# Kernel optimization log

Measured on AMD Instinct MI355X. Metric: run time of the kernel, lower is better.

The kernel has to match this reference:

```python
import jax, jax.numpy as jnp
import numpy as np

NH = 8          # attention heads
NC = 14         # disease classes
K = 10          # aspect queries per class
E = 1024        # vision_dim == text_dim
HID = 512       # hidden_dim = vision_dim // 2
TEMP = 0.1
LN_EPS = 1e-5


def _layernorm(x, g, b):
    m = jnp.mean(x, axis=-1, keepdims=True)
    v = jnp.mean(jnp.square(x - m), axis=-1, keepdims=True)
    return (x - m) * jax.lax.rsqrt(v + LN_EPS) * g + b


def _mha(q, k, v, in_w, in_b, out_w, out_b):
    # nn.MultiheadAttention (batch_first, eval mode => dropout off)
    B, Lq, Emb = q.shape
    Lk = k.shape[1]
    dh = Emb // NH
    wq, wk, wv = jnp.split(in_w, 3, axis=0)
    bq, bk, bv = jnp.split(in_b, 3)
    qh = (q @ wq.T + bq).reshape(B, Lq, NH, dh)
    kh = (k @ wk.T + bk).reshape(B, Lk, NH, dh)
    vh = (v @ wv.T + bv).reshape(B, Lk, NH, dh)
    scale = np.float32(1.0 / np.sqrt(dh))
    scores = jnp.einsum('bqhd,bkhd->bhqk', qh, kh) * scale
    attn = jax.nn.softmax(scores, axis=-1)
    out = jnp.einsum('bhqk,bkhd->bqhd', attn, vh).reshape(B, Lq, Emb)
    out = out @ out_w.T + out_b
    return out, attn.mean(axis=1)  # avg over heads, (B, Lq, Lk)


def _l2norm(x):
    return x / jnp.maximum(jnp.linalg.norm(x, axis=-1, keepdims=True), 1e-12)


def reference(vision_features, text_embeddings, vision_global, aspect_queries,
              ch_in_w, ch_in_b, ch_out_w, ch_out_b, tp_w, tp_b,
              ca_in_w, ca_in_b, ca_out_w, ca_out_b,
              cross_ln_g, cross_ln_b, cross_fc_w, cross_fc_b,
              dir_ln_g, dir_ln_b, dir_w1, dir_b1, dir_w2, dir_b2):
    B, N, _ = vision_features.shape
    # ---- contrastive branch (1-token query / 1-token kv attention) ----
    text_proj = text_embeddings @ tp_w.T + tp_b               # (B, E)
    c_out, _ = _mha(vision_global[:, None, :], text_proj[:, None, :],
                    text_proj[:, None, :], ch_in_w, ch_in_b, ch_out_w, ch_out_b)
    sim = jnp.sum(_l2norm(c_out[:, 0, :]) * _l2norm(text_proj), axis=-1) / TEMP  # (B,)
    contrastive_logits = jnp.broadcast_to(sim[:, None], (B, NC))
    # ---- supervised branch: fused per-class cross-attention (shared K/V) ----
    q = jnp.broadcast_to(aspect_queries.reshape(1, NC * K, E), (B, NC * K, E))
    att_out, attn_w = _mha(q, vision_features, vision_features,
                           ca_in_w, ca_in_b, ca_out_w, ca_out_b)
    attended = att_out.reshape(B, NC, K, E).mean(axis=2)       # (B, NC, E)
    attention_weights = attn_w.reshape(B, NC, K, N)            # (B, NC, K, N)
    # fc_cross: LN + per-class linear row (class j feature -> class j logit)
    h = _layernorm(attended, cross_ln_g, cross_ln_b)
    logits_cross = jnp.einsum('bjd,jd->bj', h, cross_fc_w) + cross_fc_b
    # fc_direct MLP on global feature
    g = _layernorm(vision_global, dir_ln_g, dir_ln_b)
    logits_direct = jax.nn.relu(g @ dir_w1.T + dir_b1) @ dir_w2.T + dir_b2
    supervised_logits = (logits_cross + logits_direct) * 0.5
    final_logits = (supervised_logits + contrastive_logits) * 0.5
    return contrastive_logits, supervised_logits, final_logits, attention_weights


def setup_inputs() -> dict:
    key = jax.random.key(0)
    ks = jax.random.split(key, 16)
    B, N = 64, 576
    w = lambda k, s: (jax.random.normal(k, s, dtype=jnp.float32) * 0.02)
    return {
        'vision_features': jax.random.normal(ks[0], (B, N, E), dtype=jnp.float32),
        'text_embeddings': jax.random.normal(ks[1], (B, E), dtype=jnp.float32),
        'vision_global': jax.random.normal(ks[2], (B, E), dtype=jnp.float32),
        'aspect_queries': jax.random.normal(ks[3], (NC, K, E), dtype=jnp.float32) / np.sqrt(E).astype(np.float32),
        'ch_in_w': w(ks[4], (3 * E, E)), 'ch_in_b': jnp.zeros((3 * E,), jnp.float32),
        'ch_out_w': w(ks[5], (E, E)), 'ch_out_b': jnp.zeros((E,), jnp.float32),
        'tp_w': w(ks[6], (E, E)), 'tp_b': jnp.zeros((E,), jnp.float32),
        'ca_in_w': w(ks[7], (3 * E, E)), 'ca_in_b': jnp.zeros((3 * E,), jnp.float32),
        'ca_out_w': w(ks[8], (E, E)), 'ca_out_b': jnp.zeros((E,), jnp.float32),
        'cross_ln_g': jnp.ones((E,), jnp.float32), 'cross_ln_b': jnp.zeros((E,), jnp.float32),
        'cross_fc_w': w(ks[9], (NC, E)), 'cross_fc_b': jnp.zeros((NC,), jnp.float32),
        'dir_ln_g': jnp.ones((E,), jnp.float32), 'dir_ln_b': jnp.zeros((E,), jnp.float32),
        'dir_w1': w(ks[10], (HID, E)), 'dir_b1': jnp.zeros((HID,), jnp.float32),
        'dir_w2': w(ks[11], (NC, HID)), 'dir_b2': jnp.zeros((NC,), jnp.float32),
    }
```

## Files before the change

kernel.cpp:

```cpp
#include <hip/hip_runtime.h>
#include <cstdio>
#include <cstdint>

using u16 = unsigned short;
typedef __bf16 bf16x8 __attribute__((ext_vector_type(8)));
typedef float f32x4 __attribute__((ext_vector_type(4)));

#define GLOBAL_AS __attribute__((address_space(1)))
#define LDS_AS __attribute__((address_space(3)))

__device__ __forceinline__ float bf2f(u16 h) {
  return __uint_as_float(((unsigned)h) << 16);
}
__device__ __forceinline__ u16 f2bf(float f) {
  unsigned u = __float_as_uint(f);
  u += 0x7FFFu + ((u >> 16) & 1u);
  return (u16)(u >> 16);
}

__device__ __forceinline__ void async_copy16(void* lds, const void* g) {
  __builtin_amdgcn_global_load_lds((const GLOBAL_AS unsigned int*)g,
                                   (LDS_AS unsigned int*)lds, 16, 0, 0);
}

__device__ __forceinline__ float block_sum(float v, float* red) {
#pragma unroll
  for (int o = 32; o >= 1; o >>= 1) v += __shfl_xor(v, o);
  __syncthreads();
  if ((threadIdx.x & 63) == 0) red[threadIdx.x >> 6] = v;
  __syncthreads();
  return red[0] + red[1] + red[2] + red[3];
}

__global__ __launch_bounds__(256) void cvt4_kernel(
    const float* __restrict__ s0, u16* __restrict__ d0,
    const float* __restrict__ s1, u16* __restrict__ d1,
    const float* __restrict__ s2, u16* __restrict__ d2,
    const float* __restrict__ s3, u16* __restrict__ d3) {
  const float* s; u16* d; long n; long b0; long nb;
  const int b = blockIdx.x;
  if (b < 2048)      { s = s0; d = d0; n = 37748736L; b0 = b;        nb = 2048; }
  else if (b < 2816) { s = s1; d = d1; n = 3145728L;  b0 = b - 2048; nb = 768; }
  else if (b < 3072) { s = s2; d = d2; n = 1048576L;  b0 = b - 2816; nb = 256; }
  else               { s = s3; d = d3; n = 143360L;   b0 = b - 3072; nb = 35; }
  long i = (b0 * 256 + threadIdx.x) * 4;
  const long stride = nb * 1024;
  for (; i < n; i += stride) {
    float4 v = *(const float4*)(s + i);
    ushort4 o;
    o.x = f2bf(v.x); o.y = f2bf(v.y); o.z = f2bf(v.z); o.w = f2bf(v.w);
    *(ushort4*)(d + i) = o;
  }
}

template <int VTD>
__global__ __launch_bounds__(512, 2) void gemm_kvq_kernel(
    const u16* __restrict__ A, const u16* __restrict__ Bkv,
    const u16* __restrict__ Aq, const u16* __restrict__ Bq,
    u16* __restrict__ Ck, u16* __restrict__ Cvp, u16* __restrict__ Vt,
    u16* __restrict__ Cq,
    const float* __restrict__ bias, const float* __restrict__ biasq) {
  __shared__ char smem[131072];
  const int bid = blockIdx.x;
  const int t = threadIdx.x;
  const int wid = t >> 6, l = t & 63;
  const int wm = wid >> 2, wn = wid & 3;
  const int lr = l & 15, lg = l >> 4, lr7 = lr & 7;

  int mt = 0, nt = 0, qb = -1;
  const u16* Abase; const u16* Bbase; const float* bias_b;
  if (bid < 1152) {
    const int wgid = (bid & 7) * 144 + (bid >> 3);
    mt = wgid >> 3; nt = wgid & 7;
    Abase = A + (size_t)mt * 256 * 1024;
    Bbase = Bkv + (size_t)nt * 256 * 1024;
    bias_b = bias + nt * 256;
  } else {
    qb = bid - 1152;
    Abase = Aq;
    Bbase = Bq + (size_t)qb * 256 * 1024;
    bias_b = biasq + qb * 256;
  }

  const int srow = t >> 3;
  const int scx = (t & 7) ^ (srow & 7);
  const char* Asrc = (const char*)Abase + (size_t)srow * 2048 + (scx << 4);
  const char* Bsrc = (const char*)Bbase + (size_t)srow * 2048 + (scx << 4);
  const int wb = wid << 10;

  f32x4 acc[8][4] = {};

#define SA(d, r, kt) async_copy16(smem + (d)*65536 + (r)*8192 + wb, \
                                  Asrc + (size_t)(r)*131072 + (size_t)(kt)*128)
#define SB(d, r, kt) async_copy16(smem + (d)*65536 + 32768 + (r)*8192 + wb, \
                                  Bsrc + (size_t)(r)*131072 + (size_t)(kt)*128)

#define RA(d, half)                                                          \
  _Pragma("unroll")                                                          \
  for (int i = 0; i < 4; ++i) {                                              \
    const int row = wm * 128 + ((half)*4 + i) * 16 + lr;                     \
    af[i][0] = *(const bf16x8*)(smem + (d)*65536 + (row << 7) + ((lg ^ lr7) << 4));       \
    af[i][1] = *(const bf16x8*)(smem + (d)*65536 + (row << 7) + (((4 | lg) ^ lr7) << 4)); \
  }

#define RB(d, half)                                                          \
  _Pragma("unroll")                                                          \
  for (int j = 0; j < 2; ++j) {                                              \
    const int row = wn * 64 + ((half)*2 + j) * 16 + lr;                      \
    bfr[j][0] = *(const bf16x8*)(smem + (d)*65536 + 32768 + (row << 7) + ((lg ^ lr7) << 4));       \
    bfr[j][1] = *(const bf16x8*)(smem + (d)*65536 + 32768 + (row << 7) + (((4 | lg) ^ lr7) << 4)); \
  }

#define MM(mh, nh)                                                           \
  __builtin_amdgcn_s_setprio(1);                                             \
  _Pragma("unroll")                                                          \
  for (int ks = 0; ks < 2; ++ks)                                             \
    _Pragma("unroll")                                                        \
    for (int i = 0; i < 4; ++i)                                              \
      _Pragma("unroll")                                                      \
      for (int j = 0; j < 2; ++j)                                            \
        acc[(mh)*4 + i][(nh)*2 + j] = __builtin_amdgcn_mfma_f32_16x16x32_bf16( \
            af[i][ks], bfr[j][ks], acc[(mh)*4 + i][(nh)*2 + j], 0, 0, 0);    \
  __builtin_amdgcn_s_setprio(0);

  SA(0, 0, 0); SA(0, 1, 0); SA(0, 2, 0); SA(0, 3, 0);
  SB(0, 0, 0); SB(0, 1, 0); SB(0, 2, 0); SB(0, 3, 0);
  SA(1, 0, 1); SA(1, 2, 1);
  asm volatile("s_waitcnt vmcnt(2)" ::: "memory");
  __builtin_amdgcn_s_barrier();
  asm volatile("" ::: "memory");

#pragma unroll 1
  for (int kt = 0; kt < 16; ++kt) {
    const int cur = kt & 1, nxt = cur ^ 1;
    const bool pf1 = (kt < 15), pf2 = (kt < 14);
    bf16x8 af[4][2], bfr[2][2];
    RA(cur, 0);
    RB(cur, 0);
    if (pf1) { SB(nxt, 0, kt + 1); SB(nxt, 1, kt + 1); }
    __builtin_amdgcn_s_barrier();
    asm volatile("s_waitcnt lgkmcnt(0)" ::: "memory");
    MM(0, 0);
    __builtin_amdgcn_s_barrier();
    RB(cur, 1);
    if (pf1) { SB(nxt, 2, kt + 1); SB(nxt, 3, kt + 1); }
    __builtin_amdgcn_s_barrier();
    asm volatile("s_waitcnt lgkmcnt(0)" ::: "memory");
    MM(0, 1);
    if (pf1) asm volatile("s_waitcnt vmcnt(6)" ::: "memory");
    __builtin_amdgcn_s_barrier();
    RA(cur, 1);
    if (pf1) { SA(nxt, 1, kt + 1); SA(nxt, 3, kt + 1); }
    __builtin_amdgcn_s_barrier();
    asm volatile("s_waitcnt lgkmcnt(0)" ::: "memory");
    MM(1, 1);
    __builtin_amdgcn_s_barrier();
    RB(cur, 0);
    if (pf2) { SA(cur, 0, kt + 2); SA(cur, 2, kt + 2); }
    __builtin_amdgcn_s_barrier();
    asm volatile("s_waitcnt lgkmcnt(0)" ::: "memory");
    MM(1, 0);
    if (pf2)      asm volatile("s_waitcnt vmcnt(4)" ::: "memory");
    else if (pf1) asm volatile("s_waitcnt vmcnt(0)" ::: "memory");
    __builtin_amdgcn_s_barrier();
  }
#undef SA
#undef SB
#undef RA
#undef RB
#undef MM

  if (VTD && qb < 0 && nt >= 4) {
    u16* T = (u16*)smem;
    const int vc2 = t >> 1, seg = t & 1;
    const int vglob = (nt - 4) * 256 + vc2;
    const int h2 = vglob >> 7, d2 = vglob & 127;
#pragma unroll 1
    for (int mh = 0; mh < 2; ++mh) {
      __syncthreads();
      if (wm == mh) {
#pragma unroll
        for (int ni = 0; ni < 4; ++ni) {
          const int vc = wn * 64 + ni * 16 + lr;
          const float bv = bias_b[vc];
#pragma unroll
          for (int mi = 0; mi < 8; ++mi) {
            const int ml = mi * 16 + lg * 4;
            ushort4 pk;
            pk.x = f2bf(acc[mi][ni][0] + bv);
            pk.y = f2bf(acc[mi][ni][1] + bv);
            pk.z = f2bf(acc[mi][ni][2] + bv);
            pk.w = f2bf(acc[mi][ni][3] + bv);
            *(ushort4*)(T + (size_t)vc * 136 + ml) = pk;
          }
        }
      }
      __syncthreads();
      const int mg0 = mt * 256 + mh * 128 + seg * 64;
      const int bb = (unsigned)mg0 / 576u;
      const int k0 = mg0 - bb * 576;
      u16* dst = Vt + ((size_t)(bb * 8 + h2) * 128 + d2) * 576 + k0;
      const u16* src = T + (size_t)vc2 * 136 + seg * 64;
#pragma unroll
      for (int i2 = 0; i2 < 8; ++i2)
        *(uint4*)(dst + i2 * 8) = *(const uint4*)(src + i2 * 8);
    }
  } else {
    u16* D; int cb0;
    if (qb >= 0)      { D = Cq;  cb0 = qb * 256; }
    else if (nt < 4)  { D = Ck;  cb0 = nt * 256; }
    else              { D = Cvp; cb0 = (nt - 4) * 256; }
#pragma unroll
    for (int ni = 0; ni < 4; ++ni) {
      const int nc = wn * 64 + ni * 16 + lr;
      const float bv = bias_b[nc];
      const int col = cb0 + nc;
#pragma unroll
      for (int mi = 0; mi < 8; ++mi) {
#pragma unroll
        for (int rg = 0; rg < 4; ++rg) {
          const size_t m = (size_t)mt * 256 + wm * 128 + mi * 16 + lg * 4 + rg;
          D[m * 1024 + col] = f2bf(acc[mi][ni][rg] + bv);
        }
      }
    }
  }
}

template <int OUTF32>
__global__ __launch_bounds__(512, 2) void gemm_big_kernel(
    const u16* __restrict__ A, const u16* __restrict__ B, void* __restrict__ Cv,
    const float* __restrict__ bias, float scale,
    int KT, int ntx, int Mlim, int Nlim,
    long lda, long ldb, long ldc, int bdiv,
    long sA0, long sA1, long sB0, long sB1, long sC0, long sC1) {
  __shared__ u16 lds[3][24576];
  const int bid = blockIdx.x;
  const int bh = blockIdx.y;
  const int bb0 = bh / bdiv, bb1 = bh % bdiv;
  const int mt = bid / ntx, nt = bid % ntx;
  const int t = threadIdx.x;
  const int wid = t >> 6, l = t & 63;
  const int wr = wid >> 1, wc = wid & 1;
  const int lr = l & 15, lg = l >> 4, lr7 = lr & 7;

  const long ldab = lda * 2, ldbb = ldb * 2;
  const u16* Abase = A + (long)bb0 * sA0 + (long)bb1 * sA1 + (long)mt * 256 * lda;
  const u16* Bbase = B + (long)bb0 * sB0 + (long)bb1 * sB1 + (long)nt * 128 * ldb;

  const int srow = t >> 3;
  const int scx = (t & 7) ^ (srow & 7);
  const char* Asrc = (const char*)Abase + (long)srow * ldab + (scx << 4);
  const char* Bsrc = (const char*)Bbase + (long)srow * ldbb + (scx << 4);
  const int wbA = wid << 10;

  char* b0 = (char*)lds[0];
  char* b1 = (char*)lds[1];
  char* b2 = (char*)lds[2];

  f32x4 acc[4][4] = {};

#define STAGE3G(dst, kt, part)                                              \
  {                                                                         \
    const long ko = (long)(kt) * 128;                                       \
    if ((part) == 0) {                                                      \
      async_copy16((dst) + wbA,          Asrc + ko);                        \
      async_copy16((dst) + 8192 + wbA,   Asrc + 64 * ldab + ko);            \
      async_copy16((dst) + 16384 + wbA,  Asrc + 128 * ldab + ko);           \
    } else {                                                                \
      async_copy16((dst) + 24576 + wbA,  Asrc + 192 * ldab + ko);           \
      async_copy16((dst) + 32768 + wbA,  Bsrc + ko);                        \
      async_copy16((dst) + 40960 + wbA,  Bsrc + 64 * ldbb + ko);            \
    }                                                                       \
  }

#define COMPUTE_KS(p, KS)                                                   \
  {                                                                         \
    const int ccol = (((KS) << 2) | lg) ^ lr7;                              \
    const char* pA = (p) + (((wr << 6) + lr) << 7) + (ccol << 4);           \
    const char* pB = (p) + 32768 + (((wc << 6) + lr) << 7) + (ccol << 4);   \
    bf16x8 af[4], bfr[4];                                                   \
    _Pragma("unroll")                                                       \
    for (int i = 0; i < 4; ++i) {                                           \
      af[i]  = *(const bf16x8*)(pA + i * 2048);                             \
      bfr[i] = *(const bf16x8*)(pB + i * 2048);                             \
    }                                                                       \
    __builtin_amdgcn_s_setprio(1);                                          \
    _Pragma("unroll")                                                       \
    for (int mi = 0; mi < 4; ++mi)                                          \
      _Pragma("unroll")                                                     \
      for (int ni = 0; ni < 4; ++ni)                                        \
        acc[mi][ni] = __builtin_amdgcn_mfma_f32_16x16x32_bf16(              \
            af[mi], bfr[ni], acc[mi][ni], 0, 0, 0);                         \
    __builtin_amdgcn_s_setprio(0);                                          \
  }

  STAGE3G(b0, 0, 0); STAGE3G(b0, 0, 1);
  STAGE3G(b1, 1, 0); STAGE3G(b1, 1, 1);
  asm volatile("s_waitcnt vmcnt(6)" ::: "memory");
  __builtin_amdgcn_s_barrier();
  asm volatile("" ::: "memory");

  char* p0 = b0; char* p1 = b1; char* p2 = b2;
#pragma unroll 1
  for (int kt = 0; kt < KT; ++kt) {
    const bool pf = (kt < KT - 2);
    if (pf) STAGE3G(p2, kt + 2, 0);
    COMPUTE_KS(p0, 0);
    if (pf) STAGE3G(p2, kt + 2, 1);
    COMPUTE_KS(p0, 1);
    if (kt < KT - 1) {
      if (pf) asm volatile("s_waitcnt vmcnt(6)" ::: "memory");
      else    asm volatile("s_waitcnt vmcnt(0)" ::: "memory");
      __builtin_amdgcn_s_barrier();
      asm volatile("" ::: "memory");
    }
    char* tmp = p0; p0 = p1; p1 = p2; p2 = tmp;
  }
#undef STAGE3G
#undef COMPUTE_KS

  const long cBase = (long)bb0 * sC0 + (long)bb1 * sC1;
  const int mr0 = mt * 256 + wr * 64 + lg * 4;
  const int nc0 = nt * 128 + wc * 64 + lr;
#pragma unroll
  for (int ni = 0; ni < 4; ++ni) {
    const int n = nc0 + ni * 16;
    if (n >= Nlim) continue;
    const float bv = bias ? bias[n] : 0.0f;
#pragma unroll
    for (int mi = 0; mi < 4; ++mi) {
#pragma unroll
      for (int rg = 0; rg < 4; ++rg) {
        const int m = mr0 + mi * 16 + rg;
        if (m >= Mlim) continue;
        const float v = acc[mi][ni][rg] * scale + bv;
        if (OUTF32) ((float*)Cv)[cBase + (long)m * ldc + n] = v;
        else        ((u16*)Cv)[cBase + (long)m * ldc + n] = f2bf(v);
      }
    }
  }
}

__global__ __launch_bounds__(256) void transpose_v_kernel(const u16* __restrict__ V,
                                                          u16* __restrict__ Vt) {
  __shared__ u16 tile[64][65];
  const int k0 = blockIdx.x * 64;
  const int c0 = blockIdx.y * 64;
  const int b = blockIdx.z;
  const int t = threadIdx.x;
  const int tx = t & 15, ty = t >> 4;
  const u16* Vb = V + (size_t)(b * 576) * 1024;
#pragma unroll
  for (int i = 0; i < 4; ++i) {
    const int k = ty + i * 16;
    const u16* src = Vb + (size_t)(k0 + k) * 1024 + c0 + tx * 4;
    ushort2 v01 = *(const ushort2*)src;
    ushort2 v23 = *(const ushort2*)(src + 2);
    tile[k][tx * 4 + 0] = v01.x; tile[k][tx * 4 + 1] = v01.y;
    tile[k][tx * 4 + 2] = v23.x; tile[k][tx * 4 + 3] = v23.y;
  }
  __syncthreads();
  const int h = c0 >> 7, d0 = c0 & 127;
  u16* VtB = Vt + ((size_t)(b * 8 + h) * 128 + d0) * 576 + k0;
#pragma unroll
  for (int i = 0; i < 4; ++i) {
    const int d = ty + i * 16;
    u16* dst = VtB + (size_t)d * 576 + tx * 4;
    ushort2 a, bb2;
    a.x = tile[tx * 4 + 0][d]; a.y = tile[tx * 4 + 1][d];
    bb2.x = tile[tx * 4 + 2][d]; bb2.y = tile[tx * 4 + 3][d];
    *(ushort2*)dst = a; *(ushort2*)(dst + 2) = bb2;
  }
}

__global__ __launch_bounds__(512) void softmax_pm_kernel(const u16* __restrict__ SP,
                                                         float* __restrict__ attnOut,
                                                         u16* __restrict__ Pm) {
  const int b = blockIdx.x, c = blockIdx.y;
  const int h = threadIdx.x >> 6, l = threadIdx.x & 63;
  __shared__ float pl[8][576];
  float pacc[9] = {};
#pragma unroll 1
  for (int qq = 0; qq < 10; ++qq) {
    const u16* row = SP + ((size_t)((b * 8 + h) * 144 + c * 10 + qq)) * 576;
    float x[9];
#pragma unroll
    for (int i = 0; i < 9; ++i) x[i] = bf2f(row[l + 64 * i]);
    float m = x[0];
#pragma unroll
    for (int i = 1; i < 9; ++i) m = fmaxf(m, x[i]);
#pragma unroll
    for (int o = 32; o >= 1; o >>= 1) m = fmaxf(m, __shfl_xor(m, o));
    float e[9], s = 0.f;
#pragma unroll
    for (int i = 0; i < 9; ++i) { e[i] = expf(x[i] - m); s += e[i]; }
#pragma unroll
    for (int o = 32; o >= 1; o >>= 1) s += __shfl_xor(s, o);
    const float inv = 1.f / s;
#pragma unroll
    for (int i = 0; i < 9; ++i) {
      const float p = e[i] * inv;
      pacc[i] += p;
      pl[h][l + 64 * i] = p;
    }
    __syncthreads();
    float* out = attnOut + ((size_t)(b * 140 + c * 10 + qq)) * 576;
    {
      const int j = threadIdx.x;
      float a = 0.f;
#pragma unroll
      for (int hh = 0; hh < 8; ++hh) a += pl[hh][j];
      out[j] = a * 0.125f;
      if (j < 64) {
        float a2 = 0.f;
#pragma unroll
        for (int hh = 0; hh < 8; ++hh) a2 += pl[hh][j + 512];
        out[j + 512] = a2 * 0.125f;
      }
    }
    __syncthreads();
  }
  u16* pm = Pm + ((size_t)((b * 8 + h) * 14 + c)) * 576;
#pragma unroll
  for (int i = 0; i < 9; ++i) pm[l + 64 * i] = f2bf(pacc[i] * 0.1f);
}

__global__ __launch_bounds__(128) void pv_small_kernel(const u16* __restrict__ Pm,
                                                       const u16* __restrict__ Vt,
                                                       u16* __restrict__ Attd) {
  const int b = blockIdx.x, hq = blockIdx.y;
  const int t = threadIdx.x;
  const int w = t >> 6, l = t & 63;
  const int h = hq * 2 + w;
  const int lr = l & 15, lg = l >> 4;
  __shared__ u16 pm[2][16][584];
  for (int i = t; i < 2336; i += 128) {
    const int hh = i / 1168;
    const int rem = i - hh * 1168;
    const int r = rem / 73, ck = rem - (rem / 73) * 73;
    uint4 v = {0u, 0u, 0u, 0u};
    if (r < 14 && ck < 72)
      v = *(const uint4*)&Pm[((size_t)((b * 8 + hq * 2 + hh) * 14 + r)) * 576 + ck * 8];
    *(uint4*)&pm[hh][r][ck * 8] = v;
  }
  __syncthreads();
  const u16* vbase = Vt + ((size_t)(b * 8 + h) * 128) * 576;
  f32x4 acc[8] = {};
#pragma unroll 1
  for (int ks = 0; ks < 18; ++ks) {
    const bf16x8 af = *(const bf16x8*)&pm[w][lr][ks * 32 + lg * 8];
#pragma unroll
    for (int nf = 0; nf < 8; ++nf) {
      const bf16x8 bf = *(const bf16x8*)&vbase[(size_t)(nf * 16 + lr) * 576 + ks * 32 + lg * 8];
      acc[nf] = __builtin_amdgcn_mfma_f32_16x16x32_bf16(af, bf, acc[nf], 0, 0, 0);
    }
  }
#pragma unroll
  for (int nf = 0; nf < 8; ++nf) {
#pragma unroll
    for (int rg = 0; rg < 4; ++rg) {
      const int cc = lg * 4 + rg;
      if (cc < 14)
        Attd[((size_t)b * 14 + cc) * 1024 + h * 128 + nf * 16 + lr] = f2bf(acc[nf][rg]);
    }
  }
}

__global__ __launch_bounds__(256) void ln_crossfc_kernel(
    const float* __restrict__ ap, const float* __restrict__ g, const float* __restrict__ bb,
    const float* __restrict__ fw, const float* __restrict__ fb, float* __restrict__ out) {
  const int bc = blockIdx.x;
  const int c = bc % 14;
  const float* x = ap + (size_t)bc * 1024;
  __shared__ float red[4];
  const int t = threadIdx.x;
  float v[4];
  float s = 0.f;
#pragma unroll
  for (int i = 0; i < 4; ++i) { v[i] = x[t + i * 256]; s += v[i]; }
  const float mean = block_sum(s, red) * (1.f / 1024.f);
  float vs = 0.f;
#pragma unroll
  for (int i = 0; i < 4; ++i) { const float d = v[i] - mean; vs += d * d; }
  const float var = block_sum(vs, red) * (1.f / 1024.f);
  const float inv = rsqrtf(var + 1e-5f);
  float acc = 0.f;
#pragma unroll
  for (int i = 0; i < 4; ++i) {
    const int e = t + i * 256;
    const float h = (v[i] - mean) * inv * g[e] + bb[e];
    acc += h * fw[(size_t)c * 1024 + e];
  }
  acc = block_sum(acc, red);
  if (t == 0) out[bc] = acc + fb[c];
}

__global__ __launch_bounds__(256) void direct_mlp_kernel(
    const float* __restrict__ vg, const float* __restrict__ g, const float* __restrict__ bb,
    const float* __restrict__ w1, const float* __restrict__ b1,
    const float* __restrict__ w2, const float* __restrict__ b2, float* __restrict__ out) {
  const int b = blockIdx.x;
  __shared__ float red[4];
  __shared__ float gn[1024];
  __shared__ float h1[512];
  const int t = threadIdx.x;
  const float* x = vg + (size_t)b * 1024;
  float v[4];
  float s = 0.f;
#pragma unroll
  for (int i = 0; i < 4; ++i) { v[i] = x[t + i * 256]; s += v[i]; }
  const float mean = block_sum(s, red) * (1.f / 1024.f);
  float vs = 0.f;
#pragma unroll
  for (int i = 0; i < 4; ++i) { const float d = v[i] - mean; vs += d * d; }
  const float var = block_sum(vs, red) * (1.f / 1024.f);
  const float inv = rsqrtf(var + 1e-5f);
#pragma unroll
  for (int i = 0; i < 4; ++i) {
    const int e = t + i * 256;
    gn[e] = (v[i] - mean) * inv * g[e] + bb[e];
  }
  __syncthreads();
  for (int j = t; j < 512; j += 256) {
    float a = b1[j];
    const float4* wr = (const float4*)(w1 + (size_t)j * 1024);
    const float4* g4 = (const float4*)gn;
    for (int e = 0; e < 256; ++e) {
      float4 wv = wr[e], av = g4[e];
      a += av.x * wv.x + av.y * wv.y + av.z * wv.z + av.w * wv.w;
    }
    h1[j] = fmaxf(a, 0.f);
  }
  __syncthreads();
  for (int c = 0; c < 14; ++c) {
    float a = 0.f;
    for (int j = t; j < 512; j += 256) a += h1[j] * w2[(size_t)c * 512 + j];
    a = block_sum(a, red);
    if (t == 0) out[b * 14 + c] = a + b2[c];
  }
}

__global__ __launch_bounds__(256) void linear_f32_kernel(
    const float* __restrict__ A, const float* __restrict__ W, const float* __restrict__ bias,
    float* __restrict__ C, int N, int Kd) {
  const int r = blockIdx.x;
  const int j = blockIdx.y * 256 + threadIdx.x;
  __shared__ float a[1024];
  for (int e = threadIdx.x; e < Kd; e += 256) a[e] = A[(size_t)r * Kd + e];
  __syncthreads();
  float acc = bias ? bias[j] : 0.f;
  const float4* wr = (const float4*)(W + (size_t)j * Kd);
  const float4* a4 = (const float4*)a;
  for (int e = 0; e < Kd / 4; ++e) {
    float4 wv = wr[e], av = a4[e];
    acc += av.x * wv.x + av.y * wv.y + av.z * wv.z + av.w * wv.w;
  }
  C[(size_t)r * N + j] = acc;
}

__global__ __launch_bounds__(256) void sim_combine_kernel(
    const float* __restrict__ co, const float* __restrict__ tp,
    const float* __restrict__ lc, const float* __restrict__ ld,
    float* __restrict__ out) {
  const int b = blockIdx.x;
  const int t = threadIdx.x;
  __shared__ float red[4];
  const float* c = co + (size_t)b * 1024;
  const float* p = tp + (size_t)b * 1024;
  float dd = 0.f, nc = 0.f, nt = 0.f;
  for (int e = t; e < 1024; e += 256) {
    const float cv = c[e], pv = p[e];
    dd += cv * pv; nc += cv * cv; nt += pv * pv;
  }
  dd = block_sum(dd, red);
  nc = block_sum(nc, red);
  nt = block_sum(nt, red);
  const float sim = dd / (fmaxf(sqrtf(nc), 1e-12f) * fmaxf(sqrtf(nt), 1e-12f)) / 0.1f;
  if (t < 14) {
    const int i = b * 14 + t;
    const float sup = 0.5f * (lc[i] + ld[i]);
    out[i] = sim;
    out[896 + i] = sup;
    out[1792 + i] = 0.5f * (sup + sim);
  }
}

static constexpr size_t OFF_X    = 0;
static constexpr size_t OFF_K    = OFF_X + 75497472;
static constexpr size_t OFF_SP   = OFF_K + 75759616;
static constexpr size_t OFF_WIN  = OFF_SP + 85082112;
static constexpr size_t OFF_WOUT = OFF_WIN + 6291456;
static constexpr size_t OFF_ASP  = OFF_WOUT + 2097152;
static constexpr size_t OFF_QASP = OFF_ASP + 524288;
static constexpr size_t OFF_ATT  = OFF_QASP + 524288;
static constexpr size_t OFF_APRJ = OFF_ATT + 1835008;
static constexpr size_t OFF_TP   = OFF_APRJ + 3670016;
static constexpr size_t OFF_CV   = OFF_TP + 262144;
static constexpr size_t OFF_CO   = OFF_CV + 262144;
static constexpr size_t OFF_SIM  = OFF_CO + 262144;
static constexpr size_t OFF_LC   = OFF_SIM + 4096;
static constexpr size_t OFF_LD   = OFF_LC + 4096;
static constexpr size_t WS_SMALL = OFF_LD + 4096;
static constexpr size_t OFF_VT   = WS_SMALL;
static constexpr size_t WS_BIG   = OFF_VT + 75497472;

extern "C" void kernel_launch(void* const* d_in, const int* in_sizes, int n_in,
                              void* d_out, int out_size, void* d_ws, size_t ws_size,
                              hipStream_t stream) {
  (void)in_sizes; (void)n_in; (void)out_size;
  const float* vision_features = (const float*)d_in[0];
  const float* text_embeddings = (const float*)d_in[1];
  const float* vision_global   = (const float*)d_in[2];
  const float* aspect_queries  = (const float*)d_in[3];
  const float* ch_in_w  = (const float*)d_in[4];
  const float* ch_in_b  = (const float*)d_in[5];
  const float* ch_out_w = (const float*)d_in[6];
  const float* ch_out_b = (const float*)d_in[7];
  const float* tp_w = (const float*)d_in[8];
  const float* tp_b = (const float*)d_in[9];
  const float* ca_in_w  = (const float*)d_in[10];
  const float* ca_in_b  = (const float*)d_in[11];
  const float* ca_out_w = (const float*)d_in[12];
  const float* ca_out_b = (const float*)d_in[13];
  const float* cross_ln_g = (const float*)d_in[14];
  const float* cross_ln_b = (const float*)d_in[15];
  const float* cross_fc_w = (const float*)d_in[16];
  const float* cross_fc_b = (const float*)d_in[17];
  const float* dir_ln_g = (const float*)d_in[18];
  const float* dir_ln_b = (const float*)d_in[19];
  const float* dir_w1 = (const float*)d_in[20];
  const float* dir_b1 = (const float*)d_in[21];
  const float* dir_w2 = (const float*)d_in[22];
  const float* dir_b2 = (const float*)d_in[23];

  if (ws_size < WS_SMALL) {
    fprintf(stderr, "kernel_launch: ws too small: %zu < %zu\n", ws_size, WS_SMALL);
    return;
  }
  const bool big = (ws_size >= WS_BIG);

  char* ws = (char*)d_ws;
  u16* Xb      = (u16*)(ws + OFF_X);
  u16* Kb      = (u16*)(ws + OFF_K);
  u16* Pm      = (u16*)(ws + OFF_K);
  u16* Vb      = (u16*)(ws + OFF_SP);
  u16* SP      = (u16*)(ws + OFF_SP);
  u16* Vt      = big ? (u16*)(ws + OFF_VT) : (u16*)(ws + OFF_X);
  u16* Win     = (u16*)(ws + OFF_WIN);
  u16* Wout    = (u16*)(ws + OFF_WOUT);
  u16* Asp     = (u16*)(ws + OFF_ASP);
  u16* Qasp    = (u16*)(ws + OFF_QASP);
  u16* Attd    = (u16*)(ws + OFF_ATT);
  float* Aprj  = (float*)(ws + OFF_APRJ);
  float* Tp    = (float*)(ws + OFF_TP);
  float* Cv2   = (float*)(ws + OFF_CV);
  float* Co    = (float*)(ws + OFF_CO);
  float* Lc    = (float*)(ws + OFF_LC);
  float* Ld    = (float*)(ws + OFF_LD);
  float* attnOut = (float*)d_out + 2688;

  cvt4_kernel<<<3107, 256, 0, stream>>>(vision_features, Xb, ca_in_w, Win,
                                        ca_out_w, Wout, aspect_queries, Asp);

  if (big) {
    gemm_kvq_kernel<1><<<dim3(1156), 512, 0, stream>>>(
        Xb, Win + 1024 * 1024, Asp, Win, Kb, nullptr, Vt, Qasp,
        ca_in_b + 1024, ca_in_b);
  } else {
    gemm_kvq_kernel<0><<<dim3(1156), 512, 0, stream>>>(
        Xb, Win + 1024 * 1024, Asp, Win, Kb, Vb, nullptr, Qasp,
        ca_in_b + 1024, ca_in_b);
    transpose_v_kernel<<<dim3(9, 16, 64), 256, 0, stream>>>(Vb, Vt);
  }

  gemm_big_kernel<0><<<dim3(5, 512), 512, 0, stream>>>(
      Qasp, Kb, SP, nullptr, 0.08838834764831845f,
      2, 5, 140, 576, 1024, 1024, 576, 8,
      0L, 128L, 589824L, 128L, 663552L, 82944L);

  softmax_pm_kernel<<<dim3(64, 14), 512, 0, stream>>>(SP, attnOut, Pm);

  pv_small_kernel<<<dim3(64, 4), 128, 0, stream>>>(Pm, Vt, Attd);

  gemm_big_kernel<1><<<dim3(32, 1), 512, 0, stream>>>(
      Attd, Wout, Aprj, ca_out_b, 1.0f,
      16, 8, 896, 1024, 1024, 1024, 1024, 1,
      0L, 0L, 0L, 0L, 0L, 0L);

  ln_crossfc_kernel<<<896, 256, 0, stream>>>(Aprj, cross_ln_g, cross_ln_b,
                                             cross_fc_w, cross_fc_b, Lc);

  direct_mlp_kernel<<<64, 256, 0, stream>>>(vision_global, dir_ln_g, dir_ln_b,
                                            dir_w1, dir_b1, dir_w2, dir_b2, Ld);

  linear_f32_kernel<<<dim3(64, 4), 256, 0, stream>>>(text_embeddings, tp_w, tp_b, Tp, 1024, 1024);
  linear_f32_kernel<<<dim3(64, 4), 256, 0, stream>>>(Tp, ch_in_w + 2048 * 1024, ch_in_b + 2048, Cv2, 1024, 1024);
  linear_f32_kernel<<<dim3(64, 4), 256, 0, stream>>>(Cv2, ch_out_w, ch_out_b, Co, 1024, 1024);

  sim_combine_kernel<<<64, 256, 0, stream>>>(Co, Tp, Lc, Ld, (float*)d_out);
}
```

Baseline: 603.5 us.

## Vectorize softmax loads, spread PV over more blocks, batch rows in small linears

The softmax kernel now reads eight contiguous bf16 scores per lane with a vector load and writes Pm in packed form, using a [72][9]-padded LDS layout for the head average. pv_small now gives each block one head, with four waves splitting the output columns, which doubles the block count. The fp32 linear kernel processes four rows per block so each weight row is reused across them, and the direct MLP computes two outputs per thread in one pass. The softmax change leaves 56 of 64 lanes idle on the tail chunk, and the linear kernels now launch far fewer blocks.

```diff
diff --git a/kernel.cpp b/kernel.cpp
--- a/kernel.cpp
+++ b/kernel.cpp
@@ -4,6 +4,7 @@
 
 using u16 = unsigned short;
 typedef __bf16 bf16x8 __attribute__((ext_vector_type(8)));
+typedef unsigned short ushort8 __attribute__((ext_vector_type(8)));
 typedef float f32x4 __attribute__((ext_vector_type(4)));
 
 #define GLOBAL_AS __attribute__((address_space(1)))
@@ -379,30 +380,49 @@
                                                          u16* __restrict__ Pm) {
   const int b = blockIdx.x, c = blockIdx.y;
   const int h = threadIdx.x >> 6, l = threadIdx.x & 63;
-  __shared__ float pl[8][576];
-  float pacc[9] = {};
+  const bool ex = (l < 8);
+  __shared__ float pl[8][72][9];
+  float pacc[16] = {};
 #pragma unroll 1
   for (int qq = 0; qq < 10; ++qq) {
     const u16* row = SP + ((size_t)((b * 8 + h) * 144 + c * 10 + qq)) * 576;
-    float x[9];
-#pragma unroll
-    for (int i = 0; i < 9; ++i) x[i] = bf2f(row[l + 64 * i]);
+    ushort8 v0 = *(const ushort8*)(row + l * 8);
+    ushort8 v1 = {0, 0, 0, 0, 0, 0, 0, 0};
+    if (ex) v1 = *(const ushort8*)(row + 512 + l * 8);
+    float x[16];
+#pragma unroll
+    for (int i = 0; i < 8; ++i) { x[i] = bf2f(v0[i]); x[8 + i] = bf2f(v1[i]); }
     float m = x[0];
 #pragma unroll
-    for (int i = 1; i < 9; ++i) m = fmaxf(m, x[i]);
+    for (int i = 1; i < 8; ++i) m = fmaxf(m, x[i]);
+    if (ex)
+#pragma unroll
+      for (int i = 8; i < 16; ++i) m = fmaxf(m, x[i]);
 #pragma unroll
     for (int o = 32; o >= 1; o >>= 1) m = fmaxf(m, __shfl_xor(m, o));
-    float e[9], s = 0.f;
-#pragma unroll
-    for (int i = 0; i < 9; ++i) { e[i] = expf(x[i] - m); s += e[i]; }
+    float e[16], s = 0.f;
+#pragma unroll
+    for (int i = 0; i < 8; ++i) { e[i] = expf(x[i] - m); s += e[i]; }
+    if (ex) {
+#pragma unroll
+      for (int i = 8; i < 16; ++i) { e[i] = expf(x[i] - m); s += e[i]; }
+    }
 #pragma unroll
     for (int o = 32; o >= 1; o >>= 1) s += __shfl_xor(s, o);
     const float inv = 1.f / s;
 #pragma unroll
-    for (int i = 0; i < 9; ++i) {
+    for (int i = 0; i < 8; ++i) {
       const float p = e[i] * inv;
       pacc[i] += p;
-      pl[h][l + 64 * i] = p;
+      pl[h][l][i] = p;
+    }
+    if (ex) {
+#pragma unroll
+      for (int i = 0; i < 8; ++i) {
+        const float p = e[8 + i] * inv;
+        pacc[8 + i] += p;
+        pl[h][64 + l][i] = p;
+      }
     }
     __syncthreads();
     float* out = attnOut + ((size_t)(b * 140 + c * 10 + qq)) * 576;
@@ -410,59 +430,72 @@
       const int j = threadIdx.x;
       float a = 0.f;
 #pragma unroll
-      for (int hh = 0; hh < 8; ++hh) a += pl[hh][j];
+      for (int hh = 0; hh < 8; ++hh) a += pl[hh][j >> 3][j & 7];
       out[j] = a * 0.125f;
       if (j < 64) {
+        const int j2 = j + 512;
         float a2 = 0.f;
 #pragma unroll
-        for (int hh = 0; hh < 8; ++hh) a2 += pl[hh][j + 512];
-        out[j + 512] = a2 * 0.125f;
+        for (int hh = 0; hh < 8; ++hh) a2 += pl[hh][j2 >> 3][j2 & 7];
+        out[j2] = a2 * 0.125f;
       }
     }
     __syncthreads();
   }
   u16* pm = Pm + ((size_t)((b * 8 + h) * 14 + c)) * 576;
-#pragma unroll
-  for (int i = 0; i < 9; ++i) pm[l + 64 * i] = f2bf(pacc[i] * 0.1f);
-}
-
-__global__ __launch_bounds__(128) void pv_small_kernel(const u16* __restrict__ Pm,
+  ushort4 pk0, pk1;
+  pk0.x = f2bf(pacc[0] * 0.1f); pk0.y = f2bf(pacc[1] * 0.1f);
+  pk0.z = f2bf(pacc[2] * 0.1f); pk0.w = f2bf(pacc[3] * 0.1f);
+  pk1.x = f2bf(pacc[4] * 0.1f); pk1.y = f2bf(pacc[5] * 0.1f);
+  pk1.z = f2bf(pacc[6] * 0.1f); pk1.w = f2bf(pacc[7] * 0.1f);
+  *(ushort4*)(pm + l * 8) = pk0;
+  *(ushort4*)(pm + l * 8 + 4) = pk1;
+  if (ex) {
+    pk0.x = f2bf(pacc[8] * 0.1f);  pk0.y = f2bf(pacc[9] * 0.1f);
+    pk0.z = f2bf(pacc[10] * 0.1f); pk0.w = f2bf(pacc[11] * 0.1f);
+    pk1.x = f2bf(pacc[12] * 0.1f); pk1.y = f2bf(pacc[13] * 0.1f);
+    pk1.z = f2bf(pacc[14] * 0.1f); pk1.w = f2bf(pacc[15] * 0.1f);
+    *(ushort4*)(pm + 512 + l * 8) = pk0;
+    *(ushort4*)(pm + 512 + l * 8 + 4) = pk1;
+  }
+}
+
+__global__ __launch_bounds__(256) void pv_small_kernel(const u16* __restrict__ Pm,
                                                        const u16* __restrict__ Vt,
                                                        u16* __restrict__ Attd) {
-  const int b = blockIdx.x, hq = blockIdx.y;
+  const int b = blockIdx.x, h = blockIdx.y;
   const int t = threadIdx.x;
   const int w = t >> 6, l = t & 63;
-  const int h = hq * 2 + w;
   const int lr = l & 15, lg = l >> 4;
-  __shared__ u16 pm[2][16][584];
-  for (int i = t; i < 2336; i += 128) {
-    const int hh = i / 1168;
-    const int rem = i - hh * 1168;
-    const int r = rem / 73, ck = rem - (rem / 73) * 73;
+  __shared__ u16 pm[16][584];
+  for (int i = t; i < 16 * 73; i += 256) {
+    const int r = i / 73, ck = i - (i / 73) * 73;
     uint4 v = {0u, 0u, 0u, 0u};
     if (r < 14 && ck < 72)
-      v = *(const uint4*)&Pm[((size_t)((b * 8 + hq * 2 + hh) * 14 + r)) * 576 + ck * 8];
-    *(uint4*)&pm[hh][r][ck * 8] = v;
+      v = *(const uint4*)&Pm[((size_t)((b * 8 + h) * 14 + r)) * 576 + ck * 8];
+    *(uint4*)&pm[r][ck * 8] = v;
   }
   __syncthreads();
   const u16* vbase = Vt + ((size_t)(b * 8 + h) * 128) * 576;
-  f32x4 acc[8] = {};
+  f32x4 acc[2] = {};
 #pragma unroll 1
   for (int ks = 0; ks < 18; ++ks) {
-    const bf16x8 af = *(const bf16x8*)&pm[w][lr][ks * 32 + lg * 8];
-#pragma unroll
-    for (int nf = 0; nf < 8; ++nf) {
+    const bf16x8 af = *(const bf16x8*)&pm[lr][ks * 32 + lg * 8];
+#pragma unroll
+    for (int j = 0; j < 2; ++j) {
+      const int nf = w * 2 + j;
       const bf16x8 bf = *(const bf16x8*)&vbase[(size_t)(nf * 16 + lr) * 576 + ks * 32 + lg * 8];
-      acc[nf] = __builtin_amdgcn_mfma_f32_16x16x32_bf16(af, bf, acc[nf], 0, 0, 0);
-    }
-  }
-#pragma unroll
-  for (int nf = 0; nf < 8; ++nf) {
+      acc[j] = __builtin_amdgcn_mfma_f32_16x16x32_bf16(af, bf, acc[j], 0, 0, 0);
+    }
+  }
+#pragma unroll
+  for (int j = 0; j < 2; ++j) {
+    const int nf = w * 2 + j;
 #pragma unroll
     for (int rg = 0; rg < 4; ++rg) {
       const int cc = lg * 4 + rg;
       if (cc < 14)
-        Attd[((size_t)b * 14 + cc) * 1024 + h * 128 + nf * 16 + lr] = f2bf(acc[nf][rg]);
+        Attd[((size_t)b * 14 + cc) * 1024 + h * 128 + nf * 16 + lr] = f2bf(acc[j][rg]);
     }
   }
 }
@@ -522,15 +555,19 @@
     gn[e] = (v[i] - mean) * inv * g[e] + bb[e];
   }
   __syncthreads();
-  for (int j = t; j < 512; j += 256) {
-    float a = b1[j];
-    const float4* wr = (const float4*)(w1 + (size_t)j * 1024);
+  {
+    float a0 = b1[t], a1 = b1[t + 256];
+    const float4* w0 = (const float4*)(w1 + (size_t)t * 1024);
+    const float4* w1p = (const float4*)(w1 + (size_t)(t + 256) * 1024);
     const float4* g4 = (const float4*)gn;
     for (int e = 0; e < 256; ++e) {
-      float4 wv = wr[e], av = g4[e];
-      a += av.x * wv.x + av.y * wv.y + av.z * wv.z + av.w * wv.w;
-    }
-    h1[j] = fmaxf(a, 0.f);
+      const float4 av = g4[e];
+      const float4 u = w0[e], q = w1p[e];
+      a0 += av.x * u.x + av.y * u.y + av.z * u.z + av.w * u.w;
+      a1 += av.x * q.x + av.y * q.y + av.z * q.z + av.w * q.w;
+    }
+    h1[t] = fmaxf(a0, 0.f);
+    h1[t + 256] = fmaxf(a1, 0.f);
   }
   __syncthreads();
   for (int c = 0; c < 14; ++c) {
@@ -543,20 +580,32 @@
 
 __global__ __launch_bounds__(256) void linear_f32_kernel(
     const float* __restrict__ A, const float* __restrict__ W, const float* __restrict__ bias,
-    float* __restrict__ C, int N, int Kd) {
-  const int r = blockIdx.x;
+    float* __restrict__ C) {
+  const int r0 = blockIdx.x * 4;
   const int j = blockIdx.y * 256 + threadIdx.x;
-  __shared__ float a[1024];
-  for (int e = threadIdx.x; e < Kd; e += 256) a[e] = A[(size_t)r * Kd + e];
+  __shared__ float a[4][1024];
+  for (int e = threadIdx.x; e < 4096; e += 256)
+    a[e >> 10][e & 1023] = A[(size_t)(r0 + (e >> 10)) * 1024 + (e & 1023)];
   __syncthreads();
-  float acc = bias ? bias[j] : 0.f;
-  const float4* wr = (const float4*)(W + (size_t)j * Kd);
-  const float4* a4 = (const float4*)a;
-  for (int e = 0; e < Kd / 4; ++e) {
-    float4 wv = wr[e], av = a4[e];
-    acc += av.x * wv.x + av.y * wv.y + av.z * wv.z + av.w * wv.w;
-  }
-  C[(size_t)r * N + j] = acc;
+  const float bv = bias ? bias[j] : 0.f;
+  float s0 = 0.f, s1 = 0.f, s2 = 0.f, s3 = 0.f;
+  const float4* wr = (const float4*)(W + (size_t)j * 1024);
+  const float4* a0 = (const float4*)a[0];
+  const float4* a1 = (const float4*)a[1];
+  const float4* a2 = (const float4*)a[2];
+  const float4* a3 = (const float4*)a[3];
+  for (int e = 0; e < 256; ++e) {
+    const float4 wv = wr[e];
+    const float4 v0 = a0[e], v1 = a1[e], v2 = a2[e], v3 = a3[e];
+    s0 += v0.x * wv.x + v0.y * wv.y + v0.z * wv.z + v0.w * wv.w;
+    s1 += v1.x * wv.x + v1.y * wv.y + v1.z * wv.z + v1.w * wv.w;
+    s2 += v2.x * wv.x + v2.y * wv.y + v2.z * wv.z + v2.w * wv.w;
+    s3 += v3.x * wv.x + v3.y * wv.y + v3.z * wv.z + v3.w * wv.w;
+  }
+  C[(size_t)(r0 + 0) * 1024 + j] = s0 + bv;
+  C[(size_t)(r0 + 1) * 1024 + j] = s1 + bv;
+  C[(size_t)(r0 + 2) * 1024 + j] = s2 + bv;
+  C[(size_t)(r0 + 3) * 1024 + j] = s3 + bv;
 }
 
 __global__ __launch_bounds__(256) void sim_combine_kernel(
@@ -681,7 +730,7 @@
 
   softmax_pm_kernel<<<dim3(64, 14), 512, 0, stream>>>(SP, attnOut, Pm);
 
-  pv_small_kernel<<<dim3(64, 4), 128, 0, stream>>>(Pm, Vt, Attd);
+  pv_small_kernel<<<dim3(64, 8), 256, 0, stream>>>(Pm, Vt, Attd);
 
   gemm_big_kernel<1><<<dim3(32, 1), 512, 0, stream>>>(
       Attd, Wout, Aprj, ca_out_b, 1.0f,
@@ -694,9 +743,9 @@
   direct_mlp_kernel<<<64, 256, 0, stream>>>(vision_global, dir_ln_g, dir_ln_b,
                                             dir_w1, dir_b1, dir_w2, dir_b2, Ld);
 
-  linear_f32_kernel<<<dim3(64, 4), 256, 0, stream>>>(text_embeddings, tp_w, tp_b, Tp, 1024, 1024);
-  linear_f32_kernel<<<dim3(64, 4), 256, 0, stream>>>(Tp, ch_in_w + 2048 * 1024, ch_in_b + 2048, Cv2, 1024, 1024);
-  linear_f32_kernel<<<dim3(64, 4), 256, 0, stream>>>(Cv2, ch_out_w, ch_out_b, Co, 1024, 1024);
+  linear_f32_kernel<<<dim3(16, 4), 256, 0, stream>>>(text_embeddings, tp_w, tp_b, Tp);
+  linear_f32_kernel<<<dim3(16, 4), 256, 0, stream>>>(Tp, ch_in_w + 2048 * 1024, ch_in_b + 2048, Cv2);
+  linear_f32_kernel<<<dim3(16, 4), 256, 0, stream>>>(Cv2, ch_out_w, ch_out_b, Co);
 
   sim_combine_kernel<<<64, 256, 0, stream>>>(Co, Tp, Lc, Ld, (float*)d_out);
 }
```

Result: slower. 695.0 us (+15.2%).
